# Performance work log

Measured on AMD Instinct MI355X. Metric: run time of the kernel, lower is better.

## Reference

```python
import jax, jax.numpy as jnp
from jax import lax
import numpy as np

T, D, DFF, E, K = 1024, 2048, 1024, 16, 6


def setup_inputs() -> dict:
    key = jax.random.key(0)
    ks = jax.random.split(key, 9)
    x = jax.random.normal(ks[0], (T, D), dtype=jnp.float32)
    selected_experts = jax.random.randint(ks[1], (T, K), 0, E, dtype=jnp.int64)
    rw = jax.random.uniform(ks[2], (T, K), dtype=jnp.float32)
    routing_weights = rw / jnp.sum(rw, axis=-1, keepdims=True)  # normalized top-k weights
    # Expert weights: w0 (gate), w1 (up): [E, DFF, D]; w2 (down): [E, D, DFF]
    w0 = jax.random.normal(ks[3], (E, DFF, D), dtype=jnp.float32) * (D ** -0.5)
    w1 = jax.random.normal(ks[4], (E, DFF, D), dtype=jnp.float32) * (D ** -0.5)
    w2 = jax.random.normal(ks[5], (E, D, DFF), dtype=jnp.float32) * (DFF ** -0.5)
    # Per-expert dequant scales (s0/s1/s2 in the fused kernel)
    s0 = jax.random.uniform(ks[6], (E,), dtype=jnp.float32, minval=0.5, maxval=1.5)
    s1 = jax.random.uniform(ks[7], (E,), dtype=jnp.float32, minval=0.5, maxval=1.5)
    s2 = jax.random.uniform(ks[8], (E,), dtype=jnp.float32, minval=0.5, maxval=1.5)
    return {"x": x, "w0": w0, "w1": w1, "w2": w2, "s0": s0, "s1": s1, "s2": s2,
            "selected_experts": selected_experts, "routing_weights": routing_weights}


def reference(x, w0, w1, w2, s0, s1, s2, selected_experts, routing_weights):
    num_experts = w0.shape[0]
    # combine weights per (token, expert): sum of routing weights over top-k slots
    onehot = jax.nn.one_hot(selected_experts, num_experts, dtype=x.dtype)  # [T,K,E]
    cw = jnp.einsum('tke,tk->et', onehot, routing_weights)                 # [E,T]

    def body(acc, inp):
        w0e, w1e, w2e, s0e, s1e, s2e, cwe = inp
        g = (x @ w0e.T) * s0e                 # [T,DFF] gate proj (dequant scale)
        u = (x @ w1e.T) * s1e                 # [T,DFF] up proj
        h = jax.nn.silu(g) * u                # SwiGLU
        y = (h @ w2e.T) * s2e                 # [T,D] down proj
        return acc + cwe[:, None] * y, None

    out, _ = lax.scan(body, jnp.zeros_like(x), (w0, w1, w2, s0, s1, s2, cw))
    return out
```

## Files before the change

### kernel.cpp

```cpp
#include <hip/hip_runtime.h>
#include <hip/hip_bf16.h>
#include <stdint.h>

#define T_TOK 1024
#define D_DIM 2048
#define DFF   1024
#define NE    16
#define TOPK  6

typedef float f32x4 __attribute__((ext_vector_type(4)));
typedef __bf16 bf16x8 __attribute__((ext_vector_type(8)));
typedef unsigned short u16x8 __attribute__((ext_vector_type(8)));
typedef unsigned int u32x4 __attribute__((ext_vector_type(4)));

__device__ __forceinline__ unsigned short f2bf(float f) {
    union { float f; unsigned int u; } v; v.f = f;
    unsigned int x = v.u;
    unsigned int r = x + 0x7FFFu + ((x >> 16) & 1u);
    return (unsigned short)(r >> 16);
}

__device__ __forceinline__ unsigned int pkbf(float a, float b) {
    unsigned int r;
    asm("v_cvt_pk_bf16_f32 %0, %1, %2" : "=v"(r) : "v"(a), "v"(b));
    return r;
}
__device__ __forceinline__ u16x8 pk8(f32x4 a, f32x4 b) {
    u32x4 r;
    r[0] = pkbf(a[0], a[1]); r[1] = pkbf(a[2], a[3]);
    r[2] = pkbf(b[0], b[1]); r[3] = pkbf(b[2], b[3]);
    return __builtin_bit_cast(u16x8, r);
}

__global__ void cvt_f32_bf16(const float* __restrict__ src,
                             unsigned short* __restrict__ dst, int n4) {
    int i = blockIdx.x * blockDim.x + threadIdx.x;
    int stride = gridDim.x * blockDim.x;
    for (; i < n4; i += stride) {
        float4 v = ((const float4*)src)[i];
        ushort4 o;
        o.x = f2bf(v.x); o.y = f2bf(v.y); o.z = f2bf(v.z); o.w = f2bf(v.w);
        ((ushort4*)dst)[i] = o;
    }
}

__global__ __launch_bounds__(1024)
void routing_kernel(const int* __restrict__ sel,
                    const float* __restrict__ rw,
                    float* __restrict__ cwl,
                    int* __restrict__ list,
                    int* __restrict__ count,
                    int* __restrict__ aoff,
                    int* __restrict__ inv) {
    __shared__ float scw[NE * T_TOK];
    __shared__ int scount[NE];
    const int t = threadIdx.x;
#pragma unroll
    for (int e = 0; e < NE; ++e) scw[e * T_TOK + t] = 0.f;
    if (t < NE) scount[t] = 0;
    __syncthreads();
#pragma unroll
    for (int k = 0; k < TOPK; ++k) {
        int e = sel[t * TOPK + k];
        scw[e * T_TOK + t] += rw[t * TOPK + k];
    }
    __syncthreads();
    int j = 0;
#pragma unroll
    for (int e = 0; e < NE; ++e) {
        float c = scw[e * T_TOK + t];
        if (c != 0.f) {
            int p = atomicAdd(&scount[e], 1);
            list[(e << 10) + p] = t;
            cwl [(e << 10) + p] = c;
            inv[t * 8 + j] = (e << 10) | p;
            ++j;
        }
    }
    for (; j < 8; ++j) inv[t * 8 + j] = -1;
    __syncthreads();
    if (t < NE) count[t] = scount[t];
    if (t == 0) {
        int o = 0;
#pragma unroll
        for (int e = 0; e < NE; ++e) { aoff[e] = o; o += (scount[e] + 127) & ~127; }
        aoff[NE] = o;
    }
}

__global__ __launch_bounds__(256, 2)
void gemm1_kernel(const unsigned short* __restrict__ xb,
                  const float* __restrict__ w0,
                  const float* __restrict__ w1,
                  const float* __restrict__ cwl,
                  const int* __restrict__ list,
                  const int* __restrict__ count,
                  const int* __restrict__ aoff,
                  const float* __restrict__ s0,
                  const float* __restrict__ s1,
                  const float* __restrict__ s2,
                  unsigned short* __restrict__ hc)
{
    const int tf = blockIdx.x, tile = blockIdx.y, e = blockIdx.z;
    const int n_e = count[e];
    const int base = tile * 128;
    if (base >= n_e) return;
    const int rowbase = aoff[e] + base;

    const int tid = threadIdx.x;
    const int lane = tid & 63, wid = tid >> 6;
    const int wm = wid >> 1, wn = wid & 1;
    const int quad = lane >> 4, l16 = lane & 15;

    __shared__ alignas(16) unsigned short sA [128 * 64];
    __shared__ alignas(16) unsigned short sB0[128 * 64];
    __shared__ alignas(16) unsigned short sB1[128 * 64];
    __shared__ int   slist[128];
    __shared__ float cws[128];

    if (tid < 128) {
        int idx = base + tid;
        int cl = idx < n_e ? idx : (n_e - 1);
        slist[tid] = list[(e << 10) + cl];
        cws[tid] = (idx < n_e) ? cwl[(e << 10) + cl] : 0.f;
    }
    __syncthreads();

    const int row0 = tid >> 3, col = tid & 7;
    const int cs = col ^ (row0 & 7);

    const float* w0e = w0 + (size_t)e * DFF * D_DIM;
    const float* w1e = w1 + (size_t)e * DFF * D_DIM;

    int iA[4], iB[4];
#pragma unroll
    for (int it = 0; it < 4; ++it) {
        int tok = slist[it * 32 + row0];
        iA[it] = tok * D_DIM + col * 8;
        iB[it] = (tf * 128 + it * 32 + row0) * D_DIM + col * 8;
    }

    f32x4 accG[4][4], accU[4][4];
    const f32x4 zz = {0.f, 0.f, 0.f, 0.f};
#pragma unroll
    for (int mi = 0; mi < 4; ++mi)
#pragma unroll
        for (int ni = 0; ni < 4; ++ni) { accG[mi][ni] = zz; accU[mi][ni] = zz; }

    u16x8 rA[4], cB0[4], cB1[4];
    f32x4 fB0[4][2], fB1[4][2];

    auto g1_load = [&](int K) {
#pragma unroll
        for (int it = 0; it < 4; ++it) {
            rA[it]     = *(const u16x8*)(xb + iA[it] + K);
            fB0[it][0] = *(const f32x4*)(w0e + iB[it] + K);
            fB0[it][1] = *(const f32x4*)(w0e + iB[it] + K + 4);
            fB1[it][0] = *(const f32x4*)(w1e + iB[it] + K);
            fB1[it][1] = *(const f32x4*)(w1e + iB[it] + K + 4);
        }
    };
    auto g1_cvt = [&]() {
#pragma unroll
        for (int it = 0; it < 4; ++it) {
            cB0[it] = pk8(fB0[it][0], fB0[it][1]);
            cB1[it] = pk8(fB1[it][0], fB1[it][1]);
        }
    };

    g1_load(0); g1_cvt();

    for (int k0 = 0; k0 < D_DIM; k0 += 64) {
        __syncthreads();
#pragma unroll
        for (int it = 0; it < 4; ++it) {
            int r = it * 32 + row0;
            *(u16x8*)(sA  + r * 64 + cs * 8) = rA[it];
            *(u16x8*)(sB0 + r * 64 + cs * 8) = cB0[it];
            *(u16x8*)(sB1 + r * 64 + cs * 8) = cB1[it];
        }
        const int k1 = k0 + 64;
        if (k1 < D_DIM) g1_load(k1);
        __syncthreads();
#pragma unroll
        for (int kk = 0; kk < 2; ++kk) {
            bf16x8 af[4];
#pragma unroll
            for (int mi = 0; mi < 4; ++mi) {
                int row = wm * 64 + mi * 16 + l16;
                int cch = (kk * 4 + quad) ^ (row & 7);
                af[mi] = __builtin_bit_cast(bf16x8,
                         *(const u16x8*)(sA + row * 64 + cch * 8));
            }
#pragma unroll
            for (int ni = 0; ni < 4; ++ni) {
                int row = wn * 64 + ni * 16 + l16;
                int cch = (kk * 4 + quad) ^ (row & 7);
                bf16x8 b0 = __builtin_bit_cast(bf16x8,
                            *(const u16x8*)(sB0 + row * 64 + cch * 8));
                bf16x8 b1 = __builtin_bit_cast(bf16x8,
                            *(const u16x8*)(sB1 + row * 64 + cch * 8));
#pragma unroll
                for (int mi = 0; mi < 4; ++mi) {
                    accG[mi][ni] = __builtin_amdgcn_mfma_f32_16x16x32_bf16(
                        af[mi], b0, accG[mi][ni], 0, 0, 0);
                    accU[mi][ni] = __builtin_amdgcn_mfma_f32_16x16x32_bf16(
                        af[mi], b1, accU[mi][ni], 0, 0, 0);
                }
            }
        }
        if (k1 < D_DIM) g1_cvt();
    }

    const float s0e = s0[e], s1e = s1[e], s2e = s2[e];
#pragma unroll
    for (int mi = 0; mi < 4; ++mi) {
#pragma unroll
        for (int reg = 0; reg < 4; ++reg) {
            int tl = wm * 64 + mi * 16 + quad * 4 + reg;
            float cwt = cws[tl] * s2e;
            size_t slot = (size_t)(rowbase + tl);
#pragma unroll
            for (int ni = 0; ni < 4; ++ni) {
                float g = accG[mi][ni][reg] * s0e;
                float u = accU[mi][ni][reg] * s1e;
                float h = g / (1.f + __expf(-g)) * u;
                int fc = tf * 128 + wn * 64 + ni * 16 + l16;
                hc[slot * DFF + fc] = f2bf(h * cwt);
            }
        }
    }
}

__global__ __launch_bounds__(256, 3)
void gemm2_kernel(const unsigned short* __restrict__ hc,
                  const float* __restrict__ w2,
                  const int* __restrict__ count,
                  const int* __restrict__ aoff,
                  float* __restrict__ hc2)
{
    const int td = blockIdx.x, tile = blockIdx.y, e = blockIdx.z;
    const int n_e = count[e];
    const int base = tile * 128;
    if (base >= n_e) return;
    const int rowbase = aoff[e] + base;

    const int tid = threadIdx.x;
    const int lane = tid & 63, wid = tid >> 6;
    const int wm = wid >> 1, wn = wid & 1;
    const int quad = lane >> 4, l16 = lane & 15;

    __shared__ alignas(16) unsigned short sA[128 * 64];
    __shared__ alignas(16) unsigned short sB[128 * 64];

    const int row0 = tid >> 3, col = tid & 7;
    const int cs = col ^ (row0 & 7);

    const float* w2e = w2 + (size_t)e * D_DIM * DFF;

    int iA[4], iB[4];
#pragma unroll
    for (int it = 0; it < 4; ++it) {
        iA[it] = (rowbase + it * 32 + row0) * DFF + col * 8;
        iB[it] = (td * 128 + it * 32 + row0) * DFF + col * 8;
    }

    f32x4 acc[4][4];
    const f32x4 zz = {0.f, 0.f, 0.f, 0.f};
#pragma unroll
    for (int mi = 0; mi < 4; ++mi)
#pragma unroll
        for (int ni = 0; ni < 4; ++ni) acc[mi][ni] = zz;

    u16x8 rA[4], cB[4];
    f32x4 fB[4][2];

    auto g2_load = [&](int K) {
#pragma unroll
        for (int it = 0; it < 4; ++it) {
            rA[it]    = *(const u16x8*)(hc + iA[it] + K);
            fB[it][0] = *(const f32x4*)(w2e + iB[it] + K);
            fB[it][1] = *(const f32x4*)(w2e + iB[it] + K + 4);
        }
    };
    auto g2_cvt = [&]() {
#pragma unroll
        for (int it = 0; it < 4; ++it) cB[it] = pk8(fB[it][0], fB[it][1]);
    };

    g2_load(0); g2_cvt();

    for (int k0 = 0; k0 < DFF; k0 += 64) {
        __syncthreads();
#pragma unroll
        for (int it = 0; it < 4; ++it) {
            int r = it * 32 + row0;
            *(u16x8*)(sA + r * 64 + cs * 8) = rA[it];
            *(u16x8*)(sB + r * 64 + cs * 8) = cB[it];
        }
        const int k1 = k0 + 64;
        if (k1 < DFF) g2_load(k1);
        __syncthreads();
#pragma unroll
        for (int kk = 0; kk < 2; ++kk) {
            bf16x8 af[4];
#pragma unroll
            for (int mi = 0; mi < 4; ++mi) {
                int row = wm * 64 + mi * 16 + l16;
                int cch = (kk * 4 + quad) ^ (row & 7);
                af[mi] = __builtin_bit_cast(bf16x8,
                         *(const u16x8*)(sA + row * 64 + cch * 8));
            }
#pragma unroll
            for (int ni = 0; ni < 4; ++ni) {
                int row = wn * 64 + ni * 16 + l16;
                int cch = (kk * 4 + quad) ^ (row & 7);
                bf16x8 bfr = __builtin_bit_cast(bf16x8,
                             *(const u16x8*)(sB + row * 64 + cch * 8));
#pragma unroll
                for (int mi = 0; mi < 4; ++mi)
                    acc[mi][ni] = __builtin_amdgcn_mfma_f32_16x16x32_bf16(
                        af[mi], bfr, acc[mi][ni], 0, 0, 0);
            }
        }
        if (k1 < DFF) g2_cvt();
    }

#pragma unroll
    for (int mi = 0; mi < 4; ++mi)
#pragma unroll
        for (int reg = 0; reg < 4; ++reg) {
            int tl = wm * 64 + mi * 16 + quad * 4 + reg;
            float* orow = hc2 + (size_t)(rowbase + tl) * D_DIM;
#pragma unroll
            for (int ni = 0; ni < 4; ++ni) {
                int d = td * 128 + wn * 64 + ni * 16 + l16;
                orow[d] = acc[mi][ni][reg];
            }
        }
}

__global__ __launch_bounds__(256)
void combine_kernel(const float* __restrict__ hc2,
                    const int* __restrict__ inv,
                    const int* __restrict__ aoff,
                    float* __restrict__ out)
{
    const int t = blockIdx.x, tid = threadIdx.x;
    __shared__ int rows[8];
    if (tid < 8) {
        int v = inv[t * 8 + tid];
        rows[tid] = (v < 0) ? -1 : (aoff[v >> 10] + (v & 1023));
    }
    __syncthreads();
    const int d0 = tid * 8;
    f32x4 a0 = {0.f, 0.f, 0.f, 0.f}, a1 = a0;
    for (int j = 0; j < 8; ++j) {
        int r = rows[j];
        if (r < 0) break;
        const f32x4* p = (const f32x4*)(hc2 + (size_t)r * D_DIM + d0);
        a0 += p[0]; a1 += p[1];
    }
    f32x4* o = (f32x4*)(out + (size_t)t * D_DIM + d0);
    o[0] = a0; o[1] = a1;
}


extern "C" void kernel_launch(void* const* d_in, const int* in_sizes, int n_in,
                              void* d_out, int out_size, void* d_ws, size_t ws_size,
                              hipStream_t stream) {
    const float* x  = (const float*)d_in[0];
    const float* w0 = (const float*)d_in[1];
    const float* w1 = (const float*)d_in[2];
    const float* w2 = (const float*)d_in[3];
    const float* s0 = (const float*)d_in[4];
    const float* s1 = (const float*)d_in[5];
    const float* s2 = (const float*)d_in[6];
    const int*   sel = (const int*)d_in[7];
    const float* rw = (const float*)d_in[8];
    float* out = (float*)d_out;

    char* ws = (char*)d_ws;
    constexpr size_t HC2_OFF  = 0;
    constexpr size_t HC_OFF   = 67108864ull;
    constexpr size_t XB_OFF   = 83886080ull;
    constexpr size_t LIST_OFF = 88080384ull;
    constexpr size_t CWL_OFF  = 88145920ull;
    constexpr size_t CNT_OFF  = 88211456ull;
    constexpr size_t AOFF_OFF = 88211712ull;
    constexpr size_t INV_OFF  = 88211968ull;
    float*          hc2   = (float*)         (ws + HC2_OFF);
    unsigned short* hc    = (unsigned short*)(ws + HC_OFF);
    unsigned short* xb    = (unsigned short*)(ws + XB_OFF);
    int*            list  = (int*)           (ws + LIST_OFF);
    float*          cwl   = (float*)         (ws + CWL_OFF);
    int*            count = (int*)           (ws + CNT_OFF);
    int*            aoff  = (int*)           (ws + AOFF_OFF);
    int*            inv   = (int*)           (ws + INV_OFF);

    routing_kernel<<<1, 1024, 0, stream>>>(sel, rw, cwl, list, count, aoff, inv);

    cvt_f32_bf16<<<2048, 256, 0, stream>>>(x, xb, T_TOK * D_DIM / 4);

    gemm1_kernel<<<dim3(DFF / 128, T_TOK / 128, NE), 256, 0, stream>>>(
        xb, w0, w1, cwl, list, count, aoff, s0, s1, s2, hc);

    gemm2_kernel<<<dim3(D_DIM / 128, T_TOK / 128, NE), 256, 0, stream>>>(
        hc, w2, count, aoff, hc2);

    combine_kernel<<<T_TOK, 256, 0, stream>>>(hc2, inv, aoff, out);
}
```

Measured before the change: 578.6 us.

## Pre-convert expert weights to bf16 and stream GEMM tiles directly into LDS

Adds a fused conversion pass that turns x, w0 and w1 into bf16, and a second pass for w2 placed between the two GEMMs. The GEMMs then read half-width weights with global_load_lds, copying 16 bytes per lane straight into swizzled LDS instead of staging through registers with in-loop f32-to-bf16 packing. gemm1's N-tile shrinks to 64 and its occupancy target rises to 3. The aim is to cut repeated fp32 weight traffic and register pressure, paid for by an extra full read and write of all weights on every call. The new loop is also single-buffered, with no register prefetch overlap, and the workspace is aliased between w0b/w2b and w1b/hc2.

Result: faster. 555.4 us (-4.0%).

```diff
diff --git a/kernel.cpp b/kernel.cpp
--- a/kernel.cpp
+++ b/kernel.cpp
@@ -11,7 +11,6 @@
 typedef float f32x4 __attribute__((ext_vector_type(4)));
 typedef __bf16 bf16x8 __attribute__((ext_vector_type(8)));
 typedef unsigned short u16x8 __attribute__((ext_vector_type(8)));
-typedef unsigned int u32x4 __attribute__((ext_vector_type(4)));
 
 __device__ __forceinline__ unsigned short f2bf(float f) {
     union { float f; unsigned int u; } v; v.f = f;
@@ -20,22 +19,38 @@
     return (unsigned short)(r >> 16);
 }
 
-__device__ __forceinline__ unsigned int pkbf(float a, float b) {
-    unsigned int r;
-    asm("v_cvt_pk_bf16_f32 %0, %1, %2" : "=v"(r) : "v"(a), "v"(b));
-    return r;
-}
-__device__ __forceinline__ u16x8 pk8(f32x4 a, f32x4 b) {
-    u32x4 r;
-    r[0] = pkbf(a[0], a[1]); r[1] = pkbf(a[2], a[3]);
-    r[2] = pkbf(b[0], b[1]); r[3] = pkbf(b[2], b[3]);
-    return __builtin_bit_cast(u16x8, r);
-}
-
-__global__ void cvt_f32_bf16(const float* __restrict__ src,
-                             unsigned short* __restrict__ dst, int n4) {
-    int i = blockIdx.x * blockDim.x + threadIdx.x;
-    int stride = gridDim.x * blockDim.x;
+typedef __attribute__((address_space(1))) const unsigned int gas_u32;
+typedef __attribute__((address_space(3))) unsigned int las_u32;
+__device__ __forceinline__ void gload16(const void* g, void* l) {
+    __builtin_amdgcn_global_load_lds((gas_u32*)g, (las_u32*)l, 16, 0, 0);
+}
+
+__global__ __launch_bounds__(256)
+void cvt3(const float* __restrict__ x,  const float* __restrict__ w0,
+          const float* __restrict__ w1,
+          unsigned short* __restrict__ xb, unsigned short* __restrict__ w0b,
+          unsigned short* __restrict__ w1b) {
+    const long NX = (long)T_TOK * D_DIM / 4;
+    const long NW = (long)NE * DFF * D_DIM / 4;
+    const long total = NX + 2 * NW;
+    long i = (long)blockIdx.x * blockDim.x + threadIdx.x;
+    const long stride = (long)gridDim.x * blockDim.x;
+    for (; i < total; i += stride) {
+        const float4* s; ushort4* d; long j;
+        if (i < NX)           { s = (const float4*)x;  d = (ushort4*)xb;  j = i; }
+        else if (i < NX + NW) { s = (const float4*)w0; d = (ushort4*)w0b; j = i - NX; }
+        else                  { s = (const float4*)w1; d = (ushort4*)w1b; j = i - NX - NW; }
+        float4 v = s[j];
+        ushort4 o;
+        o.x = f2bf(v.x); o.y = f2bf(v.y); o.z = f2bf(v.z); o.w = f2bf(v.w);
+        d[j] = o;
+    }
+}
+
+__global__ __launch_bounds__(256)
+void cvt1(const float* __restrict__ src, unsigned short* __restrict__ dst, long n4) {
+    long i = (long)blockIdx.x * blockDim.x + threadIdx.x;
+    const long stride = (long)gridDim.x * blockDim.x;
     for (; i < n4; i += stride) {
         float4 v = ((const float4*)src)[i];
         ushort4 o;
@@ -88,10 +103,10 @@
     }
 }
 
-__global__ __launch_bounds__(256, 2)
+__global__ __launch_bounds__(256, 3)
 void gemm1_kernel(const unsigned short* __restrict__ xb,
-                  const float* __restrict__ w0,
-                  const float* __restrict__ w1,
+                  const unsigned short* __restrict__ wb0,
+                  const unsigned short* __restrict__ wb1,
                   const float* __restrict__ cwl,
                   const int* __restrict__ list,
                   const int* __restrict__ count,
@@ -113,8 +128,8 @@
     const int quad = lane >> 4, l16 = lane & 15;
 
     __shared__ alignas(16) unsigned short sA [128 * 64];
-    __shared__ alignas(16) unsigned short sB0[128 * 64];
-    __shared__ alignas(16) unsigned short sB1[128 * 64];
+    __shared__ alignas(16) unsigned short sB0[64 * 64];
+    __shared__ alignas(16) unsigned short sB1[64 * 64];
     __shared__ int   slist[128];
     __shared__ float cws[128];
 
@@ -126,65 +141,48 @@
     }
     __syncthreads();
 
-    const int row0 = tid >> 3, col = tid & 7;
-    const int cs = col ^ (row0 & 7);
-
-    const float* w0e = w0 + (size_t)e * DFF * D_DIM;
-    const float* w1e = w1 + (size_t)e * DFF * D_DIM;
-
-    int iA[4], iB[4];
-#pragma unroll
-    for (int it = 0; it < 4; ++it) {
-        int tok = slist[it * 32 + row0];
-        iA[it] = tok * D_DIM + col * 8;
-        iB[it] = (tf * 128 + it * 32 + row0) * D_DIM + col * 8;
-    }
-
-    f32x4 accG[4][4], accU[4][4];
+    const int lr = lane >> 3, lc = lane & 7;
+    const int sw = lc ^ lr;
+
+    const unsigned short* w0e = wb0 + ((size_t)e * DFF + tf * 64) * D_DIM;
+    const unsigned short* w1e = wb1 + ((size_t)e * DFF + tf * 64) * D_DIM;
+
+    const unsigned short* gA[4]; int loA[4];
+    const unsigned short* gB0[2]; const unsigned short* gB1[2]; int loB[2];
+#pragma unroll
+    for (int j = 0; j < 4; ++j) {
+        int r = wid * 32 + j * 8;
+        int tok = slist[r + lr];
+        gA[j] = xb + (size_t)tok * D_DIM + sw * 8;
+        loA[j] = r * 64;
+    }
+#pragma unroll
+    for (int j = 0; j < 2; ++j) {
+        int r = wid * 16 + j * 8;
+        gB0[j] = w0e + (size_t)(r + lr) * D_DIM + sw * 8;
+        gB1[j] = w1e + (size_t)(r + lr) * D_DIM + sw * 8;
+        loB[j] = r * 64;
+    }
+
+    f32x4 accG[4][2], accU[4][2];
     const f32x4 zz = {0.f, 0.f, 0.f, 0.f};
 #pragma unroll
     for (int mi = 0; mi < 4; ++mi)
 #pragma unroll
-        for (int ni = 0; ni < 4; ++ni) { accG[mi][ni] = zz; accU[mi][ni] = zz; }
-
-    u16x8 rA[4], cB0[4], cB1[4];
-    f32x4 fB0[4][2], fB1[4][2];
-
-    auto g1_load = [&](int K) {
-#pragma unroll
-        for (int it = 0; it < 4; ++it) {
-            rA[it]     = *(const u16x8*)(xb + iA[it] + K);
-            fB0[it][0] = *(const f32x4*)(w0e + iB[it] + K);
-            fB0[it][1] = *(const f32x4*)(w0e + iB[it] + K + 4);
-            fB1[it][0] = *(const f32x4*)(w1e + iB[it] + K);
-            fB1[it][1] = *(const f32x4*)(w1e + iB[it] + K + 4);
-        }
-    };
-    auto g1_cvt = [&]() {
-#pragma unroll
-        for (int it = 0; it < 4; ++it) {
-            cB0[it] = pk8(fB0[it][0], fB0[it][1]);
-            cB1[it] = pk8(fB1[it][0], fB1[it][1]);
-        }
-    };
-
-    g1_load(0); g1_cvt();
+        for (int ni = 0; ni < 2; ++ni) { accG[mi][ni] = zz; accU[mi][ni] = zz; }
 
     for (int k0 = 0; k0 < D_DIM; k0 += 64) {
+#pragma unroll
+        for (int j = 0; j < 4; ++j) gload16(gA[j] + k0, sA + loA[j]);
+#pragma unroll
+        for (int j = 0; j < 2; ++j) {
+            gload16(gB0[j] + k0, sB0 + loB[j]);
+            gload16(gB1[j] + k0, sB1 + loB[j]);
+        }
         __syncthreads();
 #pragma unroll
-        for (int it = 0; it < 4; ++it) {
-            int r = it * 32 + row0;
-            *(u16x8*)(sA  + r * 64 + cs * 8) = rA[it];
-            *(u16x8*)(sB0 + r * 64 + cs * 8) = cB0[it];
-            *(u16x8*)(sB1 + r * 64 + cs * 8) = cB1[it];
-        }
-        const int k1 = k0 + 64;
-        if (k1 < D_DIM) g1_load(k1);
-        __syncthreads();
-#pragma unroll
         for (int kk = 0; kk < 2; ++kk) {
-            bf16x8 af[4];
+            bf16x8 af[4], b0f[2], b1f[2];
 #pragma unroll
             for (int mi = 0; mi < 4; ++mi) {
                 int row = wm * 64 + mi * 16 + l16;
@@ -193,23 +191,25 @@
                          *(const u16x8*)(sA + row * 64 + cch * 8));
             }
 #pragma unroll
-            for (int ni = 0; ni < 4; ++ni) {
-                int row = wn * 64 + ni * 16 + l16;
+            for (int ni = 0; ni < 2; ++ni) {
+                int row = wn * 32 + ni * 16 + l16;
                 int cch = (kk * 4 + quad) ^ (row & 7);
-                bf16x8 b0 = __builtin_bit_cast(bf16x8,
-                            *(const u16x8*)(sB0 + row * 64 + cch * 8));
-                bf16x8 b1 = __builtin_bit_cast(bf16x8,
-                            *(const u16x8*)(sB1 + row * 64 + cch * 8));
-#pragma unroll
-                for (int mi = 0; mi < 4; ++mi) {
+                b0f[ni] = __builtin_bit_cast(bf16x8,
+                          *(const u16x8*)(sB0 + row * 64 + cch * 8));
+                b1f[ni] = __builtin_bit_cast(bf16x8,
+                          *(const u16x8*)(sB1 + row * 64 + cch * 8));
+            }
+#pragma unroll
+            for (int mi = 0; mi < 4; ++mi)
+#pragma unroll
+                for (int ni = 0; ni < 2; ++ni) {
                     accG[mi][ni] = __builtin_amdgcn_mfma_f32_16x16x32_bf16(
-                        af[mi], b0, accG[mi][ni], 0, 0, 0);
+                        af[mi], b0f[ni], accG[mi][ni], 0, 0, 0);
                     accU[mi][ni] = __builtin_amdgcn_mfma_f32_16x16x32_bf16(
-                        af[mi], b1, accU[mi][ni], 0, 0, 0);
+                        af[mi], b1f[ni], accU[mi][ni], 0, 0, 0);
                 }
-            }
-        }
-        if (k1 < D_DIM) g1_cvt();
+        }
+        __syncthreads();
     }
 
     const float s0e = s0[e], s1e = s1[e], s2e = s2[e];
@@ -221,11 +221,11 @@
             float cwt = cws[tl] * s2e;
             size_t slot = (size_t)(rowbase + tl);
 #pragma unroll
-            for (int ni = 0; ni < 4; ++ni) {
+            for (int ni = 0; ni < 2; ++ni) {
                 float g = accG[mi][ni][reg] * s0e;
                 float u = accU[mi][ni][reg] * s1e;
                 float h = g / (1.f + __expf(-g)) * u;
-                int fc = tf * 128 + wn * 64 + ni * 16 + l16;
+                int fc = tf * 64 + wn * 32 + ni * 16 + l16;
                 hc[slot * DFF + fc] = f2bf(h * cwt);
             }
         }
@@ -234,7 +234,7 @@
 
 __global__ __launch_bounds__(256, 3)
 void gemm2_kernel(const unsigned short* __restrict__ hc,
-                  const float* __restrict__ w2,
+                  const unsigned short* __restrict__ wb2,
                   const int* __restrict__ count,
                   const int* __restrict__ aoff,
                   float* __restrict__ hc2)
@@ -253,16 +253,20 @@
     __shared__ alignas(16) unsigned short sA[128 * 64];
     __shared__ alignas(16) unsigned short sB[128 * 64];
 
-    const int row0 = tid >> 3, col = tid & 7;
-    const int cs = col ^ (row0 & 7);
-
-    const float* w2e = w2 + (size_t)e * D_DIM * DFF;
-
-    int iA[4], iB[4];
-#pragma unroll
-    for (int it = 0; it < 4; ++it) {
-        iA[it] = (rowbase + it * 32 + row0) * DFF + col * 8;
-        iB[it] = (td * 128 + it * 32 + row0) * DFF + col * 8;
+    const int lr = lane >> 3, lc = lane & 7;
+    const int sw = lc ^ lr;
+
+    const unsigned short* a_base = hc  + (size_t)rowbase * DFF;
+    const unsigned short* b_base = wb2 + ((size_t)e * D_DIM + td * 128) * DFF;
+
+    const unsigned short* gA[4]; const unsigned short* gB[4];
+    int ldso[4];
+#pragma unroll
+    for (int j = 0; j < 4; ++j) {
+        int r = wid * 32 + j * 8;
+        gA[j] = a_base + (size_t)(r + lr) * DFF + sw * 8;
+        gB[j] = b_base + (size_t)(r + lr) * DFF + sw * 8;
+        ldso[j] = r * 64;
     }
 
     f32x4 acc[4][4];
@@ -272,38 +276,16 @@
 #pragma unroll
         for (int ni = 0; ni < 4; ++ni) acc[mi][ni] = zz;
 
-    u16x8 rA[4], cB[4];
-    f32x4 fB[4][2];
-
-    auto g2_load = [&](int K) {
-#pragma unroll
-        for (int it = 0; it < 4; ++it) {
-            rA[it]    = *(const u16x8*)(hc + iA[it] + K);
-            fB[it][0] = *(const f32x4*)(w2e + iB[it] + K);
-            fB[it][1] = *(const f32x4*)(w2e + iB[it] + K + 4);
-        }
-    };
-    auto g2_cvt = [&]() {
-#pragma unroll
-        for (int it = 0; it < 4; ++it) cB[it] = pk8(fB[it][0], fB[it][1]);
-    };
-
-    g2_load(0); g2_cvt();
-
     for (int k0 = 0; k0 < DFF; k0 += 64) {
+#pragma unroll
+        for (int j = 0; j < 4; ++j) {
+            gload16(gA[j] + k0, sA + ldso[j]);
+            gload16(gB[j] + k0, sB + ldso[j]);
+        }
         __syncthreads();
 #pragma unroll
-        for (int it = 0; it < 4; ++it) {
-            int r = it * 32 + row0;
-            *(u16x8*)(sA + r * 64 + cs * 8) = rA[it];
-            *(u16x8*)(sB + r * 64 + cs * 8) = cB[it];
-        }
-        const int k1 = k0 + 64;
-        if (k1 < DFF) g2_load(k1);
-        __syncthreads();
-#pragma unroll
         for (int kk = 0; kk < 2; ++kk) {
-            bf16x8 af[4];
+            bf16x8 af[4], bfr[4];
 #pragma unroll
             for (int mi = 0; mi < 4; ++mi) {
                 int row = wm * 64 + mi * 16 + l16;
@@ -315,15 +297,17 @@
             for (int ni = 0; ni < 4; ++ni) {
                 int row = wn * 64 + ni * 16 + l16;
                 int cch = (kk * 4 + quad) ^ (row & 7);
-                bf16x8 bfr = __builtin_bit_cast(bf16x8,
-                             *(const u16x8*)(sB + row * 64 + cch * 8));
-#pragma unroll
-                for (int mi = 0; mi < 4; ++mi)
+                bfr[ni] = __builtin_bit_cast(bf16x8,
+                          *(const u16x8*)(sB + row * 64 + cch * 8));
+            }
+#pragma unroll
+            for (int mi = 0; mi < 4; ++mi)
+#pragma unroll
+                for (int ni = 0; ni < 4; ++ni)
                     acc[mi][ni] = __builtin_amdgcn_mfma_f32_16x16x32_bf16(
-                        af[mi], bfr, acc[mi][ni], 0, 0, 0);
-            }
-        }
-        if (k1 < DFF) g2_cvt();
+                        af[mi], bfr[ni], acc[mi][ni], 0, 0, 0);
+        }
+        __syncthreads();
     }
 
 #pragma unroll
@@ -381,17 +365,21 @@
     float* out = (float*)d_out;
 
     char* ws = (char*)d_ws;
-    constexpr size_t HC2_OFF  = 0;
-    constexpr size_t HC_OFF   = 67108864ull;
-    constexpr size_t XB_OFF   = 83886080ull;
-    constexpr size_t LIST_OFF = 88080384ull;
-    constexpr size_t CWL_OFF  = 88145920ull;
-    constexpr size_t CNT_OFF  = 88211456ull;
-    constexpr size_t AOFF_OFF = 88211712ull;
-    constexpr size_t INV_OFF  = 88211968ull;
-    float*          hc2   = (float*)         (ws + HC2_OFF);
+    constexpr size_t XB_OFF   = 0;
+    constexpr size_t W0B_OFF  = 4194304ull;
+    constexpr size_t W1B_OFF  = 71303168ull;
+    constexpr size_t HC_OFF   = 138412032ull;
+    constexpr size_t LIST_OFF = 155189248ull;
+    constexpr size_t CWL_OFF  = 155254784ull;
+    constexpr size_t CNT_OFF  = 155320320ull;
+    constexpr size_t AOFF_OFF = 155320576ull;
+    constexpr size_t INV_OFF  = 155320832ull;
+    unsigned short* xb    = (unsigned short*)(ws + XB_OFF);
+    unsigned short* w0b   = (unsigned short*)(ws + W0B_OFF);
+    unsigned short* w1b   = (unsigned short*)(ws + W1B_OFF);
+    unsigned short* w2b   = (unsigned short*)(ws + W0B_OFF);
     unsigned short* hc    = (unsigned short*)(ws + HC_OFF);
-    unsigned short* xb    = (unsigned short*)(ws + XB_OFF);
+    float*          hc2   = (float*)         (ws + W1B_OFF);
     int*            list  = (int*)           (ws + LIST_OFF);
     float*          cwl   = (float*)         (ws + CWL_OFF);
     int*            count = (int*)           (ws + CNT_OFF);
@@ -400,13 +388,15 @@
 
     routing_kernel<<<1, 1024, 0, stream>>>(sel, rw, cwl, list, count, aoff, inv);
 
-    cvt_f32_bf16<<<2048, 256, 0, stream>>>(x, xb, T_TOK * D_DIM / 4);
-
-    gemm1_kernel<<<dim3(DFF / 128, T_TOK / 128, NE), 256, 0, stream>>>(
-        xb, w0, w1, cwl, list, count, aoff, s0, s1, s2, hc);
+    cvt3<<<2048, 256, 0, stream>>>(x, w0, w1, xb, w0b, w1b);
+
+    gemm1_kernel<<<dim3(DFF / 64, T_TOK / 128, NE), 256, 0, stream>>>(
+        xb, w0b, w1b, cwl, list, count, aoff, s0, s1, s2, hc);
+
+    cvt1<<<2048, 256, 0, stream>>>(w2, w2b, (long)NE * D_DIM * DFF / 4);
 
     gemm2_kernel<<<dim3(D_DIM / 128, T_TOK / 128, NE), 256, 0, stream>>>(
-        hc, w2, count, aoff, hc2);
+        hc, w2b, count, aoff, hc2);
 
     combine_kernel<<<T_TOK, 256, 0, stream>>>(hc2, inv, aoff, out);
 }
```
